# Kernel optimization log

Measured on AMD Instinct MI355X. Metric: run time of the kernel, lower is better.

The kernel has to match this reference:

```python
import jax, jax.numpy as jnp
import numpy as np

N_TAGS = 64
SOS, EOS, PAD = 61, 62, 63
NEG = -1000000.0
B, S = 512, 1024


def setup_inputs() -> dict:
    key = jax.random.key(0)
    k1, k2, k3 = jax.random.split(key, 3)
    emissions = jax.random.normal(k1, (B, S, N_TAGS), dtype=jnp.float32)
    tags = jax.random.randint(k2, (B, S), 0, SOS)  # real tags only
    mask = jnp.ones((B, S), dtype=jnp.float32)
    t = jax.random.uniform(k3, (N_TAGS, N_TAGS), minval=-0.1, maxval=0.1, dtype=jnp.float32)
    t = t.at[:, SOS].set(NEG)
    t = t.at[EOS, :].set(NEG)
    t = t.at[PAD, :].set(NEG)
    t = t.at[:, PAD].set(NEG)
    t = t.at[PAD, EOS].set(0.0)
    t = t.at[PAD, PAD].set(0.0)
    return {"emissions": emissions, "tags": tags, "mask": mask, "transitions": t}


def _crf_nll(emissions, tags, mask, transitions):
    b, s, _ = emissions.shape
    # ---- gold path score (vectorized over seq) ----
    first_tags = tags[:, 0]
    last_idx = mask.astype(jnp.int32).sum(1) - 1  # [B]
    last_tags = tags[jnp.arange(b), last_idx]
    e_all = jnp.take_along_axis(emissions, tags[..., None], axis=-1)[..., 0]  # [B,S]
    t_all = transitions[tags[:, :-1], tags[:, 1:]]  # [B,S-1]
    m_tail = mask[:, 1:]
    scores = (
        transitions[SOS, first_tags]
        + e_all[:, 0]
        + jnp.sum((e_all[:, 1:] + t_all) * m_tail, axis=1)
        + transitions[last_tags, EOS]
    )
    # ---- log partition: sequential logsumexp scan ----
    alphas0 = transitions[SOS][None, :] + emissions[:, 0]  # [B,T]

    def step(alphas, inp):
        em_i, m_i = inp  # [B,T], [B]
        # scores[b, prev, cur] = alphas[b,prev] + transitions[prev,cur] + em[b,cur]
        sc = alphas[:, :, None] + transitions[None, :, :] + em_i[:, None, :]
        new_alphas = jax.nn.logsumexp(sc, axis=1)  # [B,T]
        alphas = m_i[:, None] * new_alphas + (1.0 - m_i[:, None]) * alphas
        return alphas, None

    xs = (jnp.swapaxes(emissions[:, 1:], 0, 1), jnp.swapaxes(mask[:, 1:], 0, 1))
    alphas, _ = jax.lax.scan(step, alphas0, xs)
    log_z = jax.nn.logsumexp(alphas + transitions[:, EOS][None, :], axis=1)  # [B]
    return -jnp.sum(scores - log_z)


def reference(emissions, tags, mask, transitions):
    return _crf_nll(emissions, tags, mask, transitions)
```

## Files before the change

### kernel.cpp

```cpp
#include <hip/hip_runtime.h>

#define NTAG 64
#define SOS_T 61
#define EOS_T 62
#define BB 512
#define SS 1024
#define LOG2E 1.4426950408889634f
#define LN2   0.6931471805599453f

typedef float v2f __attribute__((ext_vector_type(2)));

#define STEP(EF, MK, RESC) do {                                              \
    A_lds[j] = A;                                                            \
    const v2f* Av_ = (const v2f*)A_lds;                                      \
    v2f q0_ = {0.f, 0.f}, q1_ = q0_, q2_ = q0_, q3_ = q0_;                   \
    float mx_ = 0.f;                                                         \
    _Pragma("unroll")                                                        \
    for (int i_ = 0; i_ < 8; ++i_) {                                         \
        v2f a0_ = Av_[4*i_+0];                                               \
        v2f a1_ = Av_[4*i_+1];                                               \
        v2f a2_ = Av_[4*i_+2];                                               \
        v2f a3_ = Av_[4*i_+3];                                               \
        asm("v_pk_fma_f32 %0, %1, %2, %0" : "+v"(q0_) : "v"(a0_), "v"(expT2[4*i_+0])); \
        asm("v_pk_fma_f32 %0, %1, %2, %0" : "+v"(q1_) : "v"(a1_), "v"(expT2[4*i_+1])); \
        asm("v_pk_fma_f32 %0, %1, %2, %0" : "+v"(q2_) : "v"(a2_), "v"(expT2[4*i_+2])); \
        asm("v_pk_fma_f32 %0, %1, %2, %0" : "+v"(q3_) : "v"(a3_), "v"(expT2[4*i_+3])); \
        if (RESC) {                                                          \
            mx_ = fmaxf(mx_, fmaxf(fmaxf(a0_.x, a0_.y), fmaxf(a1_.x, a1_.y))); \
            mx_ = fmaxf(mx_, fmaxf(fmaxf(a2_.x, a2_.y), fmaxf(a3_.x, a3_.y))); \
        }                                                                    \
    }                                                                        \
    v2f qs_ = (q0_ + q1_) + (q2_ + q3_);                                     \
    float qq_ = qs_.x + qs_.y;                                               \
    float An_ = qq_ * (EF);                                                  \
    A = ((MK) != 0.f) ? An_ : A;                                             \
    if (RESC) {                                                              \
        int e_ = ((__float_as_int(mx_) >> 23) & 255) - 127;                  \
        A = ldexpf(A, -e_);                                                  \
        Mint += e_;                                                          \
    }                                                                        \
} while (0)

__global__ __launch_bounds__(64) void crf_nll_kernel(
    const float* __restrict__ emissions,
    const int*   __restrict__ tags,
    const float* __restrict__ mask,
    const float* __restrict__ trans,
    float* __restrict__ out)
{
    const int b = blockIdx.x;
    const int j = threadIdx.x;

    __shared__ __align__(16) float A_lds[NTAG];
    __shared__ __align__(16) float T_lds[NTAG * NTAG];
    __shared__ __align__(16) float mask_lds[SS];

    const float4* tg4 = (const float4*)trans;
    float4* tl4 = (float4*)T_lds;
#pragma unroll
    for (int i = 0; i < 16; ++i) tl4[i * 64 + j] = tg4[i * 64 + j];

    v2f expT2[32];
#pragma unroll
    for (int i = 0; i < 32; ++i) {
        float t0 = trans[(2 * i + 0) * NTAG + j];
        float t1 = trans[(2 * i + 1) * NTAG + j];
        expT2[i].x = exp2f(t0 * LOG2E);
        expT2[i].y = exp2f(t1 * LOG2E);
    }
    __syncthreads();

    const float* emb_g = emissions + (size_t)b * SS * NTAG;
    const int*   tgb   = tags + (size_t)b * SS;
    const float* mkb   = mask + (size_t)b * SS;

    float sc = 0.f, ms = 0.f;
#pragma unroll 4
    for (int k = 0; k < SS / 64; ++k) {
        int t = k * 64 + j;
        int tg = tgb[t];
        float m = mkb[t];
        mask_lds[t] = m;
        ms += m;
        float e = emb_g[t * NTAG + tg];
        if (t == 0) {
            sc += T_lds[SOS_T * NTAG + tg] + e;
        } else {
            int tgp = tgb[t - 1];
            sc += m * (e + T_lds[tgp * NTAG + tg]);
        }
    }
#pragma unroll
    for (int o = 32; o > 0; o >>= 1) {
        sc += __shfl_xor(sc, o);
        ms += __shfl_xor(ms, o);
    }
    int last_idx = (int)(ms + 0.5f) - 1;
    int last_tag = tgb[last_idx];
    sc += T_lds[last_tag * NTAG + EOS_T];

    float A = exp2f((T_lds[SOS_T * NTAG + j] + emb_g[j]) * LOG2E);
    int Mint = 0;

    float emr0 = emb_g[1 * NTAG + j];
    float emr1 = emb_g[2 * NTAG + j];
    float emr2 = emb_g[3 * NTAG + j];
    float emr3 = emb_g[4 * NTAG + j];
    float emr4 = emb_g[5 * NTAG + j];
    float emr5 = emb_g[6 * NTAG + j];
    float emr6 = emb_g[7 * NTAG + j];
    float emr7 = emb_g[8 * NTAG + j];

#pragma unroll 1
    for (int tb = 1; tb <= SS - 15; tb += 8) {
        float ef0 = exp2f(emr0 * LOG2E);
        float ef1 = exp2f(emr1 * LOG2E);
        float ef2 = exp2f(emr2 * LOG2E);
        float ef3 = exp2f(emr3 * LOG2E);
        float ef4 = exp2f(emr4 * LOG2E);
        float ef5 = exp2f(emr5 * LOG2E);
        float ef6 = exp2f(emr6 * LOG2E);
        float ef7 = exp2f(emr7 * LOG2E);
        float mk0 = mask_lds[tb + 0];
        float mk1 = mask_lds[tb + 1];
        float mk2 = mask_lds[tb + 2];
        float mk3 = mask_lds[tb + 3];
        float mk4 = mask_lds[tb + 4];
        float mk5 = mask_lds[tb + 5];
        float mk6 = mask_lds[tb + 6];
        float mk7 = mask_lds[tb + 7];
        int tn = tb + 8;
        emr0 = emb_g[(tn + 0) * NTAG + j];
        emr1 = emb_g[(tn + 1) * NTAG + j];
        emr2 = emb_g[(tn + 2) * NTAG + j];
        emr3 = emb_g[(tn + 3) * NTAG + j];
        emr4 = emb_g[(tn + 4) * NTAG + j];
        emr5 = emb_g[(tn + 5) * NTAG + j];
        emr6 = emb_g[(tn + 6) * NTAG + j];
        int t7 = (tn + 7 > SS - 1) ? (SS - 1) : (tn + 7);
        emr7 = emb_g[t7 * NTAG + j];

        STEP(ef0, mk0, false);
        STEP(ef1, mk1, false);
        STEP(ef2, mk2, false);
        STEP(ef3, mk3, false);
        STEP(ef4, mk4, false);
        STEP(ef5, mk5, false);
        STEP(ef6, mk6, true);
        STEP(ef7, mk7, false);
    }
    {
        float ef0 = exp2f(emr0 * LOG2E);
        float ef1 = exp2f(emr1 * LOG2E);
        float ef2 = exp2f(emr2 * LOG2E);
        float ef3 = exp2f(emr3 * LOG2E);
        float ef4 = exp2f(emr4 * LOG2E);
        float ef5 = exp2f(emr5 * LOG2E);
        float ef6 = exp2f(emr6 * LOG2E);
        STEP(ef0, mask_lds[SS - 7], false);
        STEP(ef1, mask_lds[SS - 6], false);
        STEP(ef2, mask_lds[SS - 5], true);
        STEP(ef3, mask_lds[SS - 4], false);
        STEP(ef4, mask_lds[SS - 3], false);
        STEP(ef5, mask_lds[SS - 2], false);
        STEP(ef6, mask_lds[SS - 1], false);
    }

    float val = A * exp2f(T_lds[j * NTAG + EOS_T] * LOG2E);
#pragma unroll
    for (int o = 32; o > 0; o >>= 1) val += __shfl_xor(val, o);
    float log_z = (log2f(val) + (float)Mint) * LN2;

    if (j == 0) atomicAdd(out, log_z - sc);
}

extern "C" void kernel_launch(void* const* d_in, const int* in_sizes, int n_in,
                              void* d_out, int out_size, void* d_ws, size_t ws_size,
                              hipStream_t stream) {
    const float* emissions = (const float*)d_in[0];
    const int*   tags      = (const int*)d_in[1];
    const float* mask      = (const float*)d_in[2];
    const float* trans     = (const float*)d_in[3];
    float* out = (float*)d_out;

    hipMemsetAsync(out, 0, sizeof(float), stream);
    crf_nll_kernel<<<dim3(BB), dim3(64), 0, stream>>>(emissions, tags, mask, trans, out);
}
```

Measured before the change: 325.6 us.

## Broadcast alpha vector via readlane instead of LDS round-trip per step

Each recurrence step now broadcasts the 64 alpha values across the wavefront with v_readlane into scalar registers and does 64 scalar-operand FMAs, instead of writing alpha to LDS and reading it back as packed pairs for v_pk_fma. The rescale max is taken on the raw bit patterns, and ldexp is replaced by multiplying with a constructed power of two. The time loop is unrolled to 16 steps with 16 emissions prefetched ahead. The aim is to drop LDS write/read latency from the serial dependency chain, in exchange for 64 readlanes per step, losing the packed FMA, and higher register pressure.

```diff
diff --git a/kernel.cpp b/kernel.cpp
--- a/kernel.cpp
+++ b/kernel.cpp
@@ -8,35 +8,34 @@
 #define LOG2E 1.4426950408889634f
 #define LN2   0.6931471805599453f
 
-typedef float v2f __attribute__((ext_vector_type(2)));
-
 #define STEP(EF, MK, RESC) do {                                              \
-    A_lds[j] = A;                                                            \
-    const v2f* Av_ = (const v2f*)A_lds;                                      \
-    v2f q0_ = {0.f, 0.f}, q1_ = q0_, q2_ = q0_, q3_ = q0_;                   \
-    float mx_ = 0.f;                                                         \
+    float q0_=0.f,q1_=0.f,q2_=0.f,q3_=0.f,q4_=0.f,q5_=0.f,q6_=0.f,q7_=0.f;   \
+    unsigned mxu_ = 0u;                                                      \
     _Pragma("unroll")                                                        \
-    for (int i_ = 0; i_ < 8; ++i_) {                                         \
-        v2f a0_ = Av_[4*i_+0];                                               \
-        v2f a1_ = Av_[4*i_+1];                                               \
-        v2f a2_ = Av_[4*i_+2];                                               \
-        v2f a3_ = Av_[4*i_+3];                                               \
-        asm("v_pk_fma_f32 %0, %1, %2, %0" : "+v"(q0_) : "v"(a0_), "v"(expT2[4*i_+0])); \
-        asm("v_pk_fma_f32 %0, %1, %2, %0" : "+v"(q1_) : "v"(a1_), "v"(expT2[4*i_+1])); \
-        asm("v_pk_fma_f32 %0, %1, %2, %0" : "+v"(q2_) : "v"(a2_), "v"(expT2[4*i_+2])); \
-        asm("v_pk_fma_f32 %0, %1, %2, %0" : "+v"(q3_) : "v"(a3_), "v"(expT2[4*i_+3])); \
-        if (RESC) {                                                          \
-            mx_ = fmaxf(mx_, fmaxf(fmaxf(a0_.x, a0_.y), fmaxf(a1_.x, a1_.y))); \
-            mx_ = fmaxf(mx_, fmaxf(fmaxf(a2_.x, a2_.y), fmaxf(a3_.x, a3_.y))); \
+    for (int i_ = 0; i_ < 64; ++i_) {                                        \
+        unsigned ab_ = (unsigned)__builtin_amdgcn_readlane(                  \
+                            (int)__float_as_uint(A), i_);                    \
+        float av_ = __uint_as_float(ab_);                                    \
+        switch (i_ & 7) {                                                    \
+            case 0: q0_ = fmaf(av_, eT[i_], q0_); break;                     \
+            case 1: q1_ = fmaf(av_, eT[i_], q1_); break;                     \
+            case 2: q2_ = fmaf(av_, eT[i_], q2_); break;                     \
+            case 3: q3_ = fmaf(av_, eT[i_], q3_); break;                     \
+            case 4: q4_ = fmaf(av_, eT[i_], q4_); break;                     \
+            case 5: q5_ = fmaf(av_, eT[i_], q5_); break;                     \
+            case 6: q6_ = fmaf(av_, eT[i_], q6_); break;                     \
+            default: q7_ = fmaf(av_, eT[i_], q7_); break;                    \
         }                                                                    \
+        if (RESC) mxu_ = (ab_ > mxu_) ? ab_ : mxu_;                          \
     }                                                                        \
-    v2f qs_ = (q0_ + q1_) + (q2_ + q3_);                                     \
-    float qq_ = qs_.x + qs_.y;                                               \
+    float qq_ = ((q0_+q1_)+(q2_+q3_)) + ((q4_+q5_)+(q6_+q7_));               \
     float An_ = qq_ * (EF);                                                  \
     A = ((MK) != 0.f) ? An_ : A;                                             \
     if (RESC) {                                                              \
-        int e_ = ((__float_as_int(mx_) >> 23) & 255) - 127;                  \
-        A = ldexpf(A, -e_);                                                  \
+        int e_ = (int)(mxu_ >> 23) - 127;                                    \
+        e_ = (mxu_ == 0u) ? 0 : e_;                                          \
+        float sc_ = __uint_as_float((unsigned)(127 - e_) << 23);             \
+        A *= sc_;                                                            \
         Mint += e_;                                                          \
     }                                                                        \
 } while (0)
@@ -51,7 +50,6 @@
     const int b = blockIdx.x;
     const int j = threadIdx.x;
 
-    __shared__ __align__(16) float A_lds[NTAG];
     __shared__ __align__(16) float T_lds[NTAG * NTAG];
     __shared__ __align__(16) float mask_lds[SS];
 
@@ -60,14 +58,10 @@
 #pragma unroll
     for (int i = 0; i < 16; ++i) tl4[i * 64 + j] = tg4[i * 64 + j];
 
-    v2f expT2[32];
+    float eT[NTAG];
 #pragma unroll
-    for (int i = 0; i < 32; ++i) {
-        float t0 = trans[(2 * i + 0) * NTAG + j];
-        float t1 = trans[(2 * i + 1) * NTAG + j];
-        expT2[i].x = exp2f(t0 * LOG2E);
-        expT2[i].y = exp2f(t1 * LOG2E);
-    }
+    for (int i = 0; i < NTAG; ++i)
+        eT[i] = exp2f(trans[i * NTAG + j] * LOG2E);
     __syncthreads();
 
     const float* emb_g = emissions + (size_t)b * SS * NTAG;
@@ -102,68 +96,65 @@
     float A = exp2f((T_lds[SOS_T * NTAG + j] + emb_g[j]) * LOG2E);
     int Mint = 0;
 
-    float emr0 = emb_g[1 * NTAG + j];
-    float emr1 = emb_g[2 * NTAG + j];
-    float emr2 = emb_g[3 * NTAG + j];
-    float emr3 = emb_g[4 * NTAG + j];
-    float emr4 = emb_g[5 * NTAG + j];
-    float emr5 = emb_g[6 * NTAG + j];
-    float emr6 = emb_g[7 * NTAG + j];
-    float emr7 = emb_g[8 * NTAG + j];
+    float er[16];
+#pragma unroll
+    for (int k = 0; k < 16; ++k) er[k] = emb_g[(1 + k) * NTAG + j];
 
 #pragma unroll 1
-    for (int tb = 1; tb <= SS - 15; tb += 8) {
-        float ef0 = exp2f(emr0 * LOG2E);
-        float ef1 = exp2f(emr1 * LOG2E);
-        float ef2 = exp2f(emr2 * LOG2E);
-        float ef3 = exp2f(emr3 * LOG2E);
-        float ef4 = exp2f(emr4 * LOG2E);
-        float ef5 = exp2f(emr5 * LOG2E);
-        float ef6 = exp2f(emr6 * LOG2E);
-        float ef7 = exp2f(emr7 * LOG2E);
-        float mk0 = mask_lds[tb + 0];
-        float mk1 = mask_lds[tb + 1];
-        float mk2 = mask_lds[tb + 2];
-        float mk3 = mask_lds[tb + 3];
-        float mk4 = mask_lds[tb + 4];
-        float mk5 = mask_lds[tb + 5];
-        float mk6 = mask_lds[tb + 6];
-        float mk7 = mask_lds[tb + 7];
-        int tn = tb + 8;
-        emr0 = emb_g[(tn + 0) * NTAG + j];
-        emr1 = emb_g[(tn + 1) * NTAG + j];
-        emr2 = emb_g[(tn + 2) * NTAG + j];
-        emr3 = emb_g[(tn + 3) * NTAG + j];
-        emr4 = emb_g[(tn + 4) * NTAG + j];
-        emr5 = emb_g[(tn + 5) * NTAG + j];
-        emr6 = emb_g[(tn + 6) * NTAG + j];
-        int t7 = (tn + 7 > SS - 1) ? (SS - 1) : (tn + 7);
-        emr7 = emb_g[t7 * NTAG + j];
+    for (int tb = 1; tb <= SS - 31; tb += 16) {
+        float ef[16];
+#pragma unroll
+        for (int k = 0; k < 16; ++k) ef[k] = exp2f(er[k] * LOG2E);
+#pragma unroll
+        for (int k = 0; k < 16; ++k) {
+            int tn = tb + 16 + k;
+            tn = (tn > SS - 1) ? (SS - 1) : tn;
+            er[k] = emb_g[tn * NTAG + j];
+        }
+        float mk[16];
+#pragma unroll
+        for (int k = 0; k < 16; ++k) mk[k] = mask_lds[tb + k];
 
-        STEP(ef0, mk0, false);
-        STEP(ef1, mk1, false);
-        STEP(ef2, mk2, false);
-        STEP(ef3, mk3, false);
-        STEP(ef4, mk4, false);
-        STEP(ef5, mk5, false);
-        STEP(ef6, mk6, true);
-        STEP(ef7, mk7, false);
+        STEP(ef[0],  mk[0],  false);
+        STEP(ef[1],  mk[1],  false);
+        STEP(ef[2],  mk[2],  false);
+        STEP(ef[3],  mk[3],  false);
+        STEP(ef[4],  mk[4],  false);
+        STEP(ef[5],  mk[5],  false);
+        STEP(ef[6],  mk[6],  false);
+        STEP(ef[7],  mk[7],  true);
+        STEP(ef[8],  mk[8],  false);
+        STEP(ef[9],  mk[9],  false);
+        STEP(ef[10], mk[10], false);
+        STEP(ef[11], mk[11], false);
+        STEP(ef[12], mk[12], false);
+        STEP(ef[13], mk[13], false);
+        STEP(ef[14], mk[14], false);
+        STEP(ef[15], mk[15], true);
     }
     {
-        float ef0 = exp2f(emr0 * LOG2E);
-        float ef1 = exp2f(emr1 * LOG2E);
-        float ef2 = exp2f(emr2 * LOG2E);
-        float ef3 = exp2f(emr3 * LOG2E);
-        float ef4 = exp2f(emr4 * LOG2E);
-        float ef5 = exp2f(emr5 * LOG2E);
-        float ef6 = exp2f(emr6 * LOG2E);
-        STEP(ef0, mask_lds[SS - 7], false);
-        STEP(ef1, mask_lds[SS - 6], false);
-        STEP(ef2, mask_lds[SS - 5], true);
-        STEP(ef3, mask_lds[SS - 4], false);
-        STEP(ef4, mask_lds[SS - 3], false);
-        STEP(ef5, mask_lds[SS - 2], false);
-        STEP(ef6, mask_lds[SS - 1], false);
+        float ef[15];
+#pragma unroll
+        for (int k = 0; k < 15; ++k) ef[k] = exp2f(er[k] * LOG2E);
+        float mk[15];
+#pragma unroll
+        for (int k = 0; k < 15; ++k) mk[k] = mask_lds[SS - 15 + k];
+
+        STEP(ef[0],  mk[0],  false);
+        STEP(ef[1],  mk[1],  false);
+        STEP(ef[2],  mk[2],  false);
+        STEP(ef[3],  mk[3],  false);
+        STEP(ef[4],  mk[4],  false);
+        STEP(ef[5],  mk[5],  false);
+        STEP(ef[6],  mk[6],  false);
+        STEP(ef[7],  mk[7],  true);
+        STEP(ef[8],  mk[8],  false);
+        STEP(ef[9],  mk[9],  false);
+        STEP(ef[10], mk[10], false);
+        STEP(ef[11], mk[11], false);
+        STEP(ef[12], mk[12], false);
+        STEP(ef[13], mk[13], false);
+        STEP(ef[14], mk[14], false);
     }
 
     float val = A * exp2f(T_lds[j * NTAG + EOS_T] * LOG2E);
```

Result: faster. 264.0 us (-18.9%).
